# Optimization experiments

Measured on AMD Instinct MI355X. Metric: run time of the kernel, lower is better.

Reference implementation:

```python
import jax, jax.numpy as jnp
import numpy as np


def _conv3d(x, w, stride, pad):
    return jax.lax.conv_general_dilated(
        x, w, window_strides=stride, padding=[(p, p) for p in pad],
        dimension_numbers=('NCDHW', 'OIDHW', 'NCDHW'))


def _bn(x, g, b, eps=1e-5):
    # BatchNorm3d in training mode: batch statistics over (N, D, H, W)
    m = x.mean((0, 2, 3, 4), keepdims=True)
    v = ((x - m) ** 2).mean((0, 2, 3, 4), keepdims=True)
    return (x - m) * jax.lax.rsqrt(v + eps) * g.reshape(1, -1, 1, 1, 1) + b.reshape(1, -1, 1, 1, 1)


def _lrelu(x):
    return jnp.where(x >= 0, x, 0.2 * x)


def _deform_conv3d(x, off, w, stride, pad, n_off_groups):
    # Deformable conv3d: offsets predict per-output-location (dz,dy,dx) shifts for
    # every kernel tap, shared across channel groups of size C//n_off_groups.
    B, C, D, H, W = x.shape
    O, _, kd, kh, kw = w.shape
    K = kd * kh * kw
    sd, sh, sw = stride
    pd, ph, pw = pad
    Do = (D + 2 * pd - kd) // sd + 1
    Ho = (H + 2 * ph - kh) // sh + 1
    Wo = (W + 2 * pw - kw) // sw + 1
    G = n_off_groups
    Cg = C // G
    # offset layout: [B, G, K, 3(dz,dy,dx), Do, Ho, Wo]
    off = off.reshape(B, G, K, 3, Do, Ho, Wo)
    kz, ky, kx = jnp.meshgrid(jnp.arange(kd), jnp.arange(kh), jnp.arange(kw), indexing='ij')
    bz = (jnp.arange(Do) * sd - pd).astype(x.dtype)[:, None, None]
    by = (jnp.arange(Ho) * sh - ph).astype(x.dtype)[None, :, None]
    bx = (jnp.arange(Wo) * sw - pw).astype(x.dtype)[None, None, :]
    kb = lambda a: a.reshape(-1).astype(x.dtype)[None, None, :, None, None, None]
    pz = off[:, :, :, 0] + bz + kb(kz)   # [B,G,K,Do,Ho,Wo]
    py = off[:, :, :, 1] + by + kb(ky)
    px = off[:, :, :, 2] + bx + kb(kx)
    z0, y0, x0 = jnp.floor(pz), jnp.floor(py), jnp.floor(px)
    fz, fy, fx = pz - z0, py - y0, px - x0
    xg = x.reshape(B, G, Cg, D * H * W)
    acc = jnp.zeros((B, G, Cg, K, Do, Ho, Wo), x.dtype)
    for cz in (0, 1):
        for cy in (0, 1):
            for cx in (0, 1):
                zc, yc, xc = z0 + cz, y0 + cy, x0 + cx
                wgt = ((fz if cz else 1 - fz) * (fy if cy else 1 - fy) * (fx if cx else 1 - fx))
                valid = ((zc >= 0) & (zc <= D - 1) & (yc >= 0) & (yc <= H - 1)
                         & (xc >= 0) & (xc <= W - 1)).astype(x.dtype)
                zi = jnp.clip(zc, 0, D - 1).astype(jnp.int32)
                yi = jnp.clip(yc, 0, H - 1).astype(jnp.int32)
                xi = jnp.clip(xc, 0, W - 1).astype(jnp.int32)
                idx = ((zi * H + yi) * W + xi).reshape(B, G, 1, -1)
                v = jnp.take_along_axis(xg, jnp.broadcast_to(idx, (B, G, Cg, idx.shape[-1])), axis=3)
                acc = acc + (wgt * valid)[:, :, None] * v.reshape(B, G, Cg, K, Do, Ho, Wo)
    val = acc.reshape(B, C, K, Do, Ho, Wo)
    return jnp.einsum('bckdhw,ock->bodhw', val, w.reshape(O, C, K))


def setup_inputs() -> dict:
    key = jax.random.key(0)
    ks = jax.random.split(key, 24)
    f32 = jnp.float32
    p = lambda k, shape, s=0.05: jax.random.normal(k, shape, f32) * s
    gb = lambda k, c: (1.0 + 0.05 * jax.random.normal(k, (c,), f32),
                       0.05 * jax.random.normal(jax.random.fold_in(k, 1), (c,), f32))
    g2, b2 = gb(ks[8], 64)
    g3, b3 = gb(ks[9], 128)
    g4, b4 = gb(ks[10], 256)
    g5, b5 = gb(ks[11], 512)
    g6, b6 = gb(ks[12], 512)
    return {
        'input': jax.random.normal(ks[0], (64, 3, 8, 128, 128), f32),
        'w1': p(ks[1], (32, 3, 4, 4, 4)),
        'w2': p(ks[2], (64, 32, 2, 4, 4)),
        'w3': p(ks[3], (128, 64, 2, 4, 4)),
        'w4': p(ks[4], (256, 128, 1, 4, 4)),
        'w_off': p(ks[5], (192, 256, 1, 4, 4), 0.01),
        'w5': p(ks[6], (512, 256, 1, 4, 4)),
        'w6': p(ks[7], (512, 512, 1, 4, 4)),
        'g2': g2, 'b2': b2, 'g3': g3, 'b3': b3, 'g4': g4, 'b4': b4,
        'g5': g5, 'b5': b5, 'g6': g6, 'b6': b6,
    }


def reference(input, w1, w2, w3, w4, w_off, w5, w6,
              g2, b2, g3, b3, g4, b4, g5, b5, g6, b6):
    encs = []
    out = _lrelu(_conv3d(input, w1, (2, 2, 2), (1, 1, 1)))          # norm_1 unused in forward
    encs.append(out)
    out = _lrelu(_bn(_conv3d(out, w2, (1, 2, 2), (0, 1, 1)), g2, b2))
    encs.append(out)
    out = _lrelu(_bn(_conv3d(out, w3, (1, 2, 2), (0, 1, 1)), g3, b3))
    encs.append(out)
    out = _lrelu(_bn(_conv3d(out, w4, (1, 2, 2), (0, 1, 1)), g4, b4))
    encs.append(out)
    off = _conv3d(out, w_off, (1, 2, 2), (0, 1, 1))
    out = _lrelu(_bn(_deform_conv3d(out, off, w5, (1, 2, 2), (0, 1, 1), 4), g5, b5))
    encs.append(out)
    out = _lrelu(_bn(_conv3d(out, w6, (1, 1, 1), (0, 0, 0)), g6, b6))
    encs.append(out)
    return tuple(encs)
```

## Files before the change

kernel.cpp:

```cpp
#include <hip/hip_runtime.h>
#include <hip/hip_bf16.h>
#include <cstdint>

typedef short bf16x8 __attribute__((ext_vector_type(8)));
typedef float f32x4 __attribute__((ext_vector_type(4)));

__device__ __forceinline__ float lrelu_f(float y) { return y >= 0.f ? y : 0.2f * y; }
__device__ __forceinline__ float b2f(unsigned short u) {
    union { unsigned int i; float f; } v; v.i = ((unsigned int)u) << 16; return v.f;
}
__device__ __forceinline__ unsigned short f2b(float f) {
    union { unsigned int i; float f; } v; v.f = f;
    unsigned int r = v.i + 0x7FFFu + ((v.i >> 16) & 1u);
    return (unsigned short)(r >> 16);
}

__global__ __launch_bounds__(256) void xin_cl_k(const float* __restrict__ x,
                                                unsigned short* __restrict__ xc)
{
    int i = blockIdx.x * 256 + threadIdx.x;
    int c = i & 3, w = (i >> 2) & 127, h = (i >> 9) & 127, d = (i >> 16) & 7, b = i >> 19;
    float v = (c < 3) ? x[(((size_t)b * 3 + c) * 8 + d) * 16384 + h * 128 + w] : 0.f;
    xc[i] = f2b(v);
}

__global__ __launch_bounds__(256) void repack_w(const float* __restrict__ w,
                                                unsigned short* __restrict__ wp,
                                                int Cin, int Tap, int Cip, long total)
{
    long i = (long)blockIdx.x * 256 + threadIdx.x;
    if (i >= total) return;
    int c = (int)(i % Cip);
    long t1 = i / Cip;
    int t = (int)(t1 % Tap);
    long o = t1 / Tap;
    wp[i] = (c < Cin) ? f2b(w[((size_t)o * Cin + c) * Tap + t]) : (unsigned short)0;
}

__global__ __launch_bounds__(256) void f2bk(const float* __restrict__ in,
                                            unsigned short* __restrict__ o, long n)
{
    long i = (long)blockIdx.x * 256 + threadIdx.x;
    if (i < n) o[i] = f2b(in[i]);
}

template<int BN, int AMODE, int EPI>
__global__ __launch_bounds__(256) void igemm(
    const unsigned short* __restrict__ A, const unsigned short* __restrict__ Bw,
    void* __restrict__ Cout,
    int M, int N, int K, int klen,
    int Ci, int Di, int Hi, int Wi,
    int kd, int kh, int kw,
    int sd, int sh_, int sw_, int pd, int ph_, int pw_,
    int Do, int Ho, int Wo)
{
    constexpr int NF = BN / 32;
    constexpr int WN = 16 * NF;
    constexpr int NBU = (BN * 4 + 255) / 256;
    __shared__ __align__(16) unsigned short As[4][128][8];
    __shared__ __align__(16) unsigned short Bs[4][BN][8];
    const int tid = threadIdx.x;
    const int m0 = blockIdx.x * 128;
    const int n0 = blockIdx.y * BN;
    const int k0 = blockIdx.z * klen;
    const int kend = min(K, k0 + klen);

    size_t bsrc[NBU];
    unsigned short* bdst[NBU];
#pragma unroll
    for (int i = 0; i < NBU; ++i) {
        int u = tid + i * 256;
        int row = u >> 2, s = u & 3;
        if (BN * 4 >= 256 || u < BN * 4) {
            bsrc[i] = (size_t)(n0 + row) * K + s * 8;
            bdst[i] = &Bs[s][row][0];
        }
    }

    constexpr int NAU = (AMODE == 2) ? 4 : 2;
    size_t asz[2];
    int asrc[NAU];
    unsigned long long amask[NAU];
    unsigned short* adst[NAU];

    if constexpr (AMODE == 0) {
#pragma unroll
        for (int i = 0; i < 2; ++i) {
            int u = tid + i * 256;
            int r = u >> 2, s = u & 3;
            asz[i] = (size_t)(m0 + r) * K + s * 8;
            adst[i] = &As[s][r][0];
        }
    } else {
#pragma unroll
        for (int i = 0; i < NAU; ++i) {
            int u = tid + i * 256;
            int r = (AMODE == 2) ? (u >> 3) : (u >> 2);
            int m = m0 + r;
            int ow = m % Wo; int t1 = m / Wo;
            int oh = t1 % Ho; t1 /= Ho;
            int od = t1 % Do; int b = t1 / Do;
            int id0 = od * sd - pd, ih0 = oh * sh_ - ph_, iw0 = ow * sw_ - pw_;
            unsigned long long xm = 0ull, yx = 0ull, mask = 0ull;
            for (int p = 0; p < kw; ++p) if ((unsigned)(iw0 + p) < (unsigned)Wi) xm |= 1ull << p;
            for (int p = 0; p < kh; ++p) if ((unsigned)(ih0 + p) < (unsigned)Hi) yx |= xm << (p * kw);
            for (int p = 0; p < kd; ++p) if ((unsigned)(id0 + p) < (unsigned)Di) mask |= yx << (p * kh * kw);
            amask[i] = mask;
            int bsp = ((b * Di + id0) * Hi + ih0) * Wi + iw0;
            if constexpr (AMODE == 1) {
                int s = u & 3;
                asrc[i] = bsp * Ci + s * 8;
                adst[i] = &As[s][r][0];
            } else {
                int j = u & 7;
                asrc[i] = (bsp + (j >> 2) * Wi + (j & 3)) * 4;
                adst[i] = &As[j >> 1][r][(j & 1) * 4];
            }
        }
    }

    f32x4 acc[4][NF];
#pragma unroll
    for (int i = 0; i < 4; ++i)
#pragma unroll
        for (int j = 0; j < NF; ++j) acc[i][j] = (f32x4){0.f, 0.f, 0.f, 0.f};

    const int lane = tid & 63, wv = tid >> 6;
    const int wm = wv >> 1, wn = wv & 1;
    const int kg = lane >> 4, fr = lane & 15;

    int c0 = 0, kx = 0, ky = 0, tap = 0, doff = 0;
    if constexpr (AMODE == 1) {
        c0 = k0 % Ci;
        tap = k0 / Ci;
        kx = tap % kw;
        int t2 = tap / kw;
        ky = t2 % kh;
        int kz = t2 / kh;
        doff = (kz * Hi + ky) * Wi + kx;
    }

    for (int k = k0; k < kend; k += 32) {
#pragma unroll
        for (int i = 0; i < NBU; ++i)
            if (BN * 4 >= 256 || tid + i * 256 < BN * 4) {
                uint4 v = *(const uint4*)&Bw[bsrc[i] + k];
                *(uint4*)bdst[i] = v;
            }
        if constexpr (AMODE == 0) {
#pragma unroll
            for (int i = 0; i < 2; ++i) {
                uint4 v = *(const uint4*)&A[asz[i] + k];
                *(uint4*)adst[i] = v;
            }
        } else if constexpr (AMODE == 1) {
            int dofe = doff * Ci + c0;
#pragma unroll
            for (int i = 0; i < 2; ++i) {
                uint4 v = {0u, 0u, 0u, 0u};
                if ((amask[i] >> tap) & 1ull)
                    v = *(const uint4*)&A[(size_t)(asrc[i] + dofe)];
                *(uint4*)adst[i] = v;
            }
        } else {
            int kz = k >> 6;
            int U4 = (kz * (Hi * Wi) + ((k >> 5) & 1) * 2 * Wi) * 4;
            int tap0 = k >> 2;
#pragma unroll
            for (int i = 0; i < 4; ++i) {
                int j = (tid + i * 256) & 7;
                uint2 v = {0u, 0u};
                if ((amask[i] >> (tap0 + j)) & 1ull)
                    v = *(const uint2*)&A[(size_t)(asrc[i] + U4)];
                *(uint2*)adst[i] = v;
            }
        }
        __syncthreads();
        bf16x8 af[4], bfr[NF];
#pragma unroll
        for (int mi = 0; mi < 4; ++mi)
            af[mi] = *(const bf16x8*)&As[kg][wm * 64 + mi * 16 + fr][0];
#pragma unroll
        for (int ni = 0; ni < NF; ++ni)
            bfr[ni] = *(const bf16x8*)&Bs[kg][wn * WN + ni * 16 + fr][0];
#pragma unroll
        for (int mi = 0; mi < 4; ++mi)
#pragma unroll
            for (int ni = 0; ni < NF; ++ni)
                acc[mi][ni] = __builtin_amdgcn_mfma_f32_16x16x32_bf16(af[mi], bfr[ni], acc[mi][ni], 0, 0, 0);
        __syncthreads();
        if constexpr (AMODE == 1) {
            c0 += 32;
            if (c0 >= Ci) {
                c0 = 0; ++tap; ++kx; ++doff;
                if (kx == kw) {
                    kx = 0; doff += Wi - kw; ++ky;
                    if (ky == kh) { ky = 0; doff += (Hi - kh) * Wi; }
                }
            }
        }
    }
    const int rb = m0 + wm * 64 + (lane >> 4) * 4;
    const int cb = n0 + wn * WN + fr;
#pragma unroll
    for (int mi = 0; mi < 4; ++mi)
#pragma unroll
        for (int ni = 0; ni < NF; ++ni)
#pragma unroll
            for (int rg = 0; rg < 4; ++rg) {
                size_t idx = (size_t)(rb + mi * 16 + rg) * N + cb + ni * 16;
                float vv = acc[mi][ni][rg];
                if constexpr (EPI == 0) ((unsigned short*)Cout)[idx] = f2b(vv);
                else if constexpr (EPI == 1) ((float*)Cout)[idx] = vv;
                else if constexpr (EPI == 2) atomicAdd((float*)Cout + idx, vv);
                else ((unsigned short*)Cout)[idx] = f2b(lrelu_f(vv));
            }
}

__global__ __launch_bounds__(256) void bn_sums(const unsigned short* __restrict__ x,
                                               float* __restrict__ sums,
                                               long totalSlots, int C)
{
    const int tid = threadIdx.x;
    long gid = (long)blockIdx.x * 256 + tid;
    long stride = (long)gridDim.x * 256;
    float s1[8], s2[8];
#pragma unroll
    for (int j = 0; j < 8; ++j) { s1[j] = 0.f; s2[j] = 0.f; }
    for (long s = gid; s < totalSlots; s += stride) {
        uint4 v = *(const uint4*)&x[s * 8];
        const unsigned short* pv = (const unsigned short*)&v;
#pragma unroll
        for (int j = 0; j < 8; ++j) { float f = b2f(pv[j]); s1[j] += f; s2[j] += f * f; }
    }
    __shared__ float r1[2048], r2[2048];
#pragma unroll
    for (int j = 0; j < 8; ++j) { r1[tid * 8 + j] = s1[j]; r2[tid * 8 + j] = s2[j]; }
    __syncthreads();
    int G = C >> 3;
    for (int c = tid; c < C; c += 256) {
        int grp = c >> 3, j = c & 7;
        float a = 0.f, b = 0.f;
        for (int th = grp; th < 256; th += G) { a += r1[th * 8 + j]; b += r2[th * 8 + j]; }
        atomicAdd(&sums[c], a);
        atomicAdd(&sums[C + c], b);
    }
}

__global__ __launch_bounds__(256) void bn_fin(const float* __restrict__ sums,
                                              const float* __restrict__ g, const float* __restrict__ bt,
                                              float* __restrict__ sc, float* __restrict__ sh,
                                              int C, float invcnt)
{
    int c = blockIdx.x * 256 + threadIdx.x;
    if (c >= C) return;
    float mean = sums[c] * invcnt;
    float var = sums[C + c] * invcnt - mean * mean;
    float rs = rsqrtf(var + 1e-5f);
    float scl = g[c] * rs;
    sc[c] = scl;
    sh[c] = bt[c] - mean * scl;
}

template<int MODE>
__global__ __launch_bounds__(256) void bn_apply_t(
    unsigned short* __restrict__ x, const float* __restrict__ sc, const float* __restrict__ sh,
    float* __restrict__ outN, int C, int TC, int S)
{
    __shared__ __align__(16) float T[64][68];
    const int tid = threadIdx.x;
    const long m0 = (long)blockIdx.x * 64;
    const int c0 = blockIdx.y * TC;
    const int spr = TC >> 3;
    const int lg = (spr == 8) ? 3 : 2;
    const int tot = 64 * spr;
    for (int u = tid; u < tot; u += 256) {
        int r = u >> lg, sl = u & (spr - 1);
        size_t idx = (size_t)(m0 + r) * C + c0 + sl * 8;
        uint4 v = *(uint4*)&x[idx];
        unsigned short* pv = (unsigned short*)&v;
#pragma unroll
        for (int j = 0; j < 8; ++j) {
            int c = c0 + sl * 8 + j;
            float f = b2f(pv[j]);
            if (MODE == 1) {
                f = lrelu_f(f * sc[c] + sh[c]);
                pv[j] = f2b(f);
            }
            T[sl * 8 + j][r] = f;
        }
        if (MODE == 1) *(uint4*)&x[idx] = v;
    }
    __syncthreads();
    const int tpc = 256 / TC;
    const int rpt = 64 / tpc;
    int cl = tid / tpc;
    int r0 = (tid % tpc) * rpt;
    int c = c0 + cl;
    if ((S & 63) == 0) {
        long b = m0 / S;
        long s0 = m0 - b * S;
        float* op = outN + ((size_t)b * C + c) * S + s0 + r0;
        for (int r = 0; r < rpt; r += 4)
            *(float4*)(op + r) = *(float4*)&T[cl][r0 + r];
    } else {
        for (int r = 0; r < rpt; ++r) {
            long m = m0 + r0 + r;
            long b = m / S, s = m - b * S;
            outN[((size_t)b * C + c) * S + s] = T[cl][r0 + r];
        }
    }
}

__global__ __launch_bounds__(256) void deform_val(
    const unsigned short* __restrict__ xcl, const float* __restrict__ offc,
    unsigned short* __restrict__ val)
{
    int bs = blockIdx.x;
    int b = bs >> 5, s = bs & 31;
    int od = s >> 4, oh = (s >> 2) & 3, ow = s & 3;
    __shared__ float cw[64][8];
    __shared__ int cidx[64][8];
    int tid = threadIdx.x;
    if (tid < 64) {
        int gk = tid, k = gk & 15;
        int ky = k >> 2, kx = k & 3;
        const float* op = offc + (size_t)bs * 192 + gk * 3;
        float pz = op[0] + (float)od;
        float py = op[1] + (float)(oh * 2 - 1 + ky);
        float px = op[2] + (float)(ow * 2 - 1 + kx);
        float z0 = floorf(pz), y0 = floorf(py), x0 = floorf(px);
        float fz = pz - z0, fy = py - y0, fx = px - x0;
#pragma unroll
        for (int ci = 0; ci < 8; ++ci) {
            int cz = ci >> 2, cy = (ci >> 1) & 1, cx = ci & 1;
            float zc = z0 + cz, yc = y0 + cy, xc = x0 + cx;
            bool ok = zc >= 0.f && zc <= 1.f && yc >= 0.f && yc <= 7.f && xc >= 0.f && xc <= 7.f;
            int zi = min(max((int)zc, 0), 1);
            int yi = min(max((int)yc, 0), 7);
            int xi = min(max((int)xc, 0), 7);
            float wz = cz ? fz : 1.f - fz;
            float wy = cy ? fy : 1.f - fy;
            float wx = cx ? fx : 1.f - fx;
            cw[gk][ci] = ok ? wz * wy * wx : 0.f;
            cidx[gk][ci] = (zi * 8 + yi) * 8 + xi;
        }
    }
    __syncthreads();
    const unsigned short* xb = xcl + (size_t)b * 128 * 256;
    unsigned short* vo = val + (size_t)bs * 4096;
    for (int j = tid; j < 4096; j += 256) {
        int c = j & 255, tap = j >> 8;
        int gk = ((c >> 6) << 4) | tap;
        float v = 0.f;
#pragma unroll
        for (int i = 0; i < 8; ++i)
            v += cw[gk][i] * b2f(xb[(size_t)cidx[gk][i] * 256 + c]);
        vo[j] = f2b(v);
    }
}

extern "C" void kernel_launch(void* const* d_in, const int* in_sizes, int n_in,
                              void* d_out, int out_size, void* d_ws, size_t ws_size,
                              hipStream_t stream)
{
    (void)in_sizes; (void)n_in; (void)out_size; (void)ws_size;
    const float* x     = (const float*)d_in[0];
    const float* w1    = (const float*)d_in[1];
    const float* w2    = (const float*)d_in[2];
    const float* w3    = (const float*)d_in[3];
    const float* w4    = (const float*)d_in[4];
    const float* w_off = (const float*)d_in[5];
    const float* w5    = (const float*)d_in[6];
    const float* w6    = (const float*)d_in[7];
    const float* g2 = (const float*)d_in[8];  const float* b2 = (const float*)d_in[9];
    const float* g3 = (const float*)d_in[10]; const float* b3 = (const float*)d_in[11];
    const float* g4 = (const float*)d_in[12]; const float* b4 = (const float*)d_in[13];
    const float* g5 = (const float*)d_in[14]; const float* b5 = (const float*)d_in[15];
    const float* g6 = (const float*)d_in[16]; const float* b6 = (const float*)d_in[17];

    float* out = (float*)d_out;
    float* enc0 = out;
    float* enc1 = out + 33554432;
    float* enc2 = out + 46137344;
    float* enc3 = out + 50331648;
    float* enc4 = out + 52428800;
    float* enc5 = out + 53477376;

    char* W = (char*)d_ws;
    unsigned short* w1p  = (unsigned short*)(W + 0);
    unsigned short* w2p  = (unsigned short*)(W + 16384);
    unsigned short* w3p  = (unsigned short*)(W + 147456);
    unsigned short* w4p  = (unsigned short*)(W + 671744);
    unsigned short* wofp = (unsigned short*)(W + 1720320);
    unsigned short* w5p  = (unsigned short*)(W + 3293184);
    unsigned short* w6p  = (unsigned short*)(W + 7487488);
    float* sums          = (float*)(W + 15876096);
    float* sc            = (float*)(W + 15880192);
    float* sh            = (float*)(W + 15882240);
    float* offc          = (float*)(W + 15884288);
    unsigned short* xcl  = (unsigned short*)(W + 17457152);
    unsigned short* e1c  = (unsigned short*)(W + 17457152);
    unsigned short* e2c  = (unsigned short*)(W + 42622976);
    unsigned short* e3c  = (unsigned short*)(W + 51011584);
    unsigned short* e0c  = (unsigned short*)(W + 84566016);
    unsigned short* valb = (unsigned short*)(W + 84566016);
    float* raw5          = (float*)(W + 101343232);
    unsigned short* e4c  = (unsigned short*)(W + 105537536);
    float* raw6          = (float*)(W + 107634688);
    unsigned short* e5c  = (unsigned short*)(W + 107896832);

    xin_cl_k<<<131072, 256, 0, stream>>>(x, xcl);
    repack_w<<<32, 256, 0, stream>>>(w1, w1p, 3, 64, 4, 8192L);
    repack_w<<<256, 256, 0, stream>>>(w2, w2p, 32, 32, 32, 65536L);
    repack_w<<<1024, 256, 0, stream>>>(w3, w3p, 64, 32, 64, 262144L);
    repack_w<<<2048, 256, 0, stream>>>(w4, w4p, 128, 16, 128, 524288L);
    repack_w<<<3072, 256, 0, stream>>>(w_off, wofp, 256, 16, 256, 786432L);
    repack_w<<<8192, 256, 0, stream>>>(w5, w5p, 256, 16, 256, 2097152L);
    repack_w<<<16384, 256, 0, stream>>>(w6, w6p, 512, 16, 512, 4194304L);

    igemm<32, 2, 3><<<dim3(8192, 1, 1), 256, 0, stream>>>(
        xcl, w1p, e0c, 1048576, 32, 256, 256,
        4, 8, 128, 128, 4, 4, 4, 2, 2, 2, 1, 1, 1, 4, 64, 64);
    bn_apply_t<0><<<dim3(16384, 1), 256, 0, stream>>>(e0c, nullptr, nullptr, enc0, 32, 32, 16384);

    igemm<64, 1, 0><<<dim3(1536, 1, 1), 256, 0, stream>>>(
        e0c, w2p, e1c, 196608, 64, 1024, 1024,
        32, 4, 64, 64, 2, 4, 4, 1, 2, 2, 0, 1, 1, 3, 32, 32);
    hipMemsetAsync(sums, 0, 4096, stream);
    bn_sums<<<256, 256, 0, stream>>>(e1c, sums, 1572864L, 64);
    bn_fin<<<1, 256, 0, stream>>>(sums, g2, b2, sc, sh, 64, 1.f / 196608.f);
    bn_apply_t<1><<<dim3(3072, 1), 256, 0, stream>>>(e1c, sc, sh, enc1, 64, 64, 3072);

    igemm<128, 1, 0><<<dim3(256, 1, 1), 256, 0, stream>>>(
        e1c, w3p, e2c, 32768, 128, 2048, 2048,
        64, 3, 32, 32, 2, 4, 4, 1, 2, 2, 0, 1, 1, 2, 16, 16);
    hipMemsetAsync(sums, 0, 4096, stream);
    bn_sums<<<256, 256, 0, stream>>>(e2c, sums, 524288L, 128);
    bn_fin<<<1, 256, 0, stream>>>(sums, g3, b3, sc, sh, 128, 1.f / 32768.f);
    bn_apply_t<1><<<dim3(512, 2), 256, 0, stream>>>(e2c, sc, sh, enc2, 128, 64, 512);

    igemm<64, 1, 0><<<dim3(64, 4), 256, 0, stream>>>(
        e2c, w4p, e3c, 8192, 256, 2048, 2048,
        128, 2, 16, 16, 1, 4, 4, 1, 2, 2, 0, 1, 1, 2, 8, 8);
    hipMemsetAsync(sums, 0, 4096, stream);
    bn_sums<<<256, 256, 0, stream>>>(e3c, sums, 262144L, 256);
    bn_fin<<<1, 256, 0, stream>>>(sums, g4, b4, sc, sh, 256, 1.f / 8192.f);
    bn_apply_t<1><<<dim3(128, 4), 256, 0, stream>>>(e3c, sc, sh, enc3, 256, 64, 128);

    hipMemsetAsync(offc, 0, 1572864, stream);
    igemm<64, 1, 2><<<dim3(16, 3, 8), 256, 0, stream>>>(
        e3c, wofp, offc, 2048, 192, 4096, 512,
        256, 2, 8, 8, 1, 4, 4, 1, 2, 2, 0, 1, 1, 2, 4, 4);

    deform_val<<<2048, 256, 0, stream>>>(e3c, offc, valb);
    hipMemsetAsync(raw5, 0, 4194304, stream);
    igemm<64, 0, 2><<<dim3(16, 8, 4), 256, 0, stream>>>(
        valb, w5p, raw5, 2048, 512, 4096, 1024,
        0, 0, 0, 0, 1, 1, 1, 1, 1, 1, 0, 0, 0, 1, 1, 1);
    f2bk<<<4096, 256, 0, stream>>>(raw5, e4c, 1048576L);
    hipMemsetAsync(sums, 0, 4096, stream);
    bn_sums<<<256, 256, 0, stream>>>(e4c, sums, 131072L, 512);
    bn_fin<<<2, 256, 0, stream>>>(sums, g5, b5, sc, sh, 512, 1.f / 2048.f);
    bn_apply_t<1><<<dim3(32, 8), 256, 0, stream>>>(e4c, sc, sh, enc4, 512, 64, 32);

    hipMemsetAsync(raw6, 0, 262144, stream);
    igemm<64, 0, 2><<<dim3(1, 8, 16), 256, 0, stream>>>(
        e4c, w6p, raw6, 128, 512, 8192, 512,
        0, 0, 0, 0, 1, 1, 1, 1, 1, 1, 0, 0, 0, 1, 1, 1);
    f2bk<<<256, 256, 0, stream>>>(raw6, e5c, 65536L);
    hipMemsetAsync(sums, 0, 4096, stream);
    bn_sums<<<256, 256, 0, stream>>>(e5c, sums, 8192L, 512);
    bn_fin<<<2, 256, 0, stream>>>(sums, g6, b6, sc, sh, 512, 1.f / 128.f);
    bn_apply_t<1><<<dim3(2, 8), 256, 0, stream>>>(e5c, sc, sh, enc5, 512, 64, 2);
}
```

Measured before the change: 650.2 us.

## Fuse BN statistics into GEMM epilogue, merge weight repacks, unroll K by 64

The seven weight-repack launches become one kernel. BN sum and sum-of-squares are now accumulated in the igemm epilogue (new EPI mode 4), using shared-memory reduction and then global atomics, which removes the separate bn_sums passes and most memsets; bn_fin now zeroes the sums for the next layer. The f32-to-bf16 conversion and the stats are fused into one pass for the split-K layers. The GEMM main loop now stages two 32-wide K slices per sync, halving barriers, and the split-K factor is doubled for layers 5 and 6. In exchange it uses more shared memory per block and adds atomic contention in the epilogue, and the BN stats are now computed from fp32 values rather than from the rounded bf16 outputs.

```diff
diff --git a/kernel.cpp b/kernel.cpp
--- a/kernel.cpp
+++ b/kernel.cpp
@@ -24,30 +24,32 @@
     xc[i] = f2b(v);
 }
 
-__global__ __launch_bounds__(256) void repack_w(const float* __restrict__ w,
-                                                unsigned short* __restrict__ wp,
-                                                int Cin, int Tap, int Cip, long total)
+__global__ __launch_bounds__(256) void repack_all(
+    const float* __restrict__ w1, const float* __restrict__ w2,
+    const float* __restrict__ w3, const float* __restrict__ w4,
+    const float* __restrict__ w_off, const float* __restrict__ w5,
+    const float* __restrict__ w6, unsigned short* __restrict__ wp)
 {
     long i = (long)blockIdx.x * 256 + threadIdx.x;
-    if (i >= total) return;
-    int c = (int)(i % Cip);
-    long t1 = i / Cip;
+    const float* src; int Cin, Tap, Cip; long rel;
+    if (i < 8192)         { src = w1;    Cin = 3;   Tap = 64; Cip = 4;   rel = i; }
+    else if (i < 73728)   { src = w2;    Cin = 32;  Tap = 32; Cip = 32;  rel = i - 8192; }
+    else if (i < 335872)  { src = w3;    Cin = 64;  Tap = 32; Cip = 64;  rel = i - 73728; }
+    else if (i < 860160)  { src = w4;    Cin = 128; Tap = 16; Cip = 128; rel = i - 335872; }
+    else if (i < 1646592) { src = w_off; Cin = 256; Tap = 16; Cip = 256; rel = i - 860160; }
+    else if (i < 3743744) { src = w5;    Cin = 256; Tap = 16; Cip = 256; rel = i - 1646592; }
+    else                  { src = w6;    Cin = 512; Tap = 16; Cip = 512; rel = i - 3743744; }
+    int c = (int)(rel % Cip);
+    long t1 = rel / Cip;
     int t = (int)(t1 % Tap);
     long o = t1 / Tap;
-    wp[i] = (c < Cin) ? f2b(w[((size_t)o * Cin + c) * Tap + t]) : (unsigned short)0;
-}
-
-__global__ __launch_bounds__(256) void f2bk(const float* __restrict__ in,
-                                            unsigned short* __restrict__ o, long n)
-{
-    long i = (long)blockIdx.x * 256 + threadIdx.x;
-    if (i < n) o[i] = f2b(in[i]);
+    wp[i] = (c < Cin) ? f2b(src[((size_t)o * Cin + c) * Tap + t]) : (unsigned short)0;
 }
 
 template<int BN, int AMODE, int EPI>
 __global__ __launch_bounds__(256) void igemm(
     const unsigned short* __restrict__ A, const unsigned short* __restrict__ Bw,
-    void* __restrict__ Cout,
+    void* __restrict__ Cout, float* __restrict__ sums,
     int M, int N, int K, int klen,
     int Ci, int Di, int Hi, int Wi,
     int kd, int kh, int kw,
@@ -57,31 +59,36 @@
     constexpr int NF = BN / 32;
     constexpr int WN = 16 * NF;
     constexpr int NBU = (BN * 4 + 255) / 256;
-    __shared__ __align__(16) unsigned short As[4][128][8];
-    __shared__ __align__(16) unsigned short Bs[4][BN][8];
+    constexpr int NAU = (AMODE == 2) ? 4 : 2;
+    constexpr int ASTR = 4 * 128 * 8;
+    constexpr int BSTR = 4 * BN * 8;
+    __shared__ __align__(16) unsigned short As[2][4][128][8];
+    __shared__ __align__(16) unsigned short Bs[2][4][BN][8];
+    __shared__ float redbuf[(EPI == 4) ? 2 * BN : 1];
     const int tid = threadIdx.x;
     const int m0 = blockIdx.x * 128;
     const int n0 = blockIdx.y * BN;
     const int k0 = blockIdx.z * klen;
     const int kend = min(K, k0 + klen);
+    unsigned short* const As0 = &As[0][0][0][0];
+    unsigned short* const Bs0 = &Bs[0][0][0][0];
 
     size_t bsrc[NBU];
-    unsigned short* bdst[NBU];
+    int boff[NBU];
 #pragma unroll
     for (int i = 0; i < NBU; ++i) {
         int u = tid + i * 256;
         int row = u >> 2, s = u & 3;
         if (BN * 4 >= 256 || u < BN * 4) {
             bsrc[i] = (size_t)(n0 + row) * K + s * 8;
-            bdst[i] = &Bs[s][row][0];
-        }
-    }
-
-    constexpr int NAU = (AMODE == 2) ? 4 : 2;
+            boff[i] = (s * BN + row) * 8;
+        }
+    }
+
     size_t asz[2];
     int asrc[NAU];
     unsigned long long amask[NAU];
-    unsigned short* adst[NAU];
+    int aoff[NAU];
 
     if constexpr (AMODE == 0) {
 #pragma unroll
@@ -89,7 +96,7 @@
             int u = tid + i * 256;
             int r = u >> 2, s = u & 3;
             asz[i] = (size_t)(m0 + r) * K + s * 8;
-            adst[i] = &As[s][r][0];
+            aoff[i] = (s * 128 + r) * 8;
         }
     } else {
 #pragma unroll
@@ -110,11 +117,11 @@
             if constexpr (AMODE == 1) {
                 int s = u & 3;
                 asrc[i] = bsp * Ci + s * 8;
-                adst[i] = &As[s][r][0];
+                aoff[i] = (s * 128 + r) * 8;
             } else {
                 int j = u & 7;
                 asrc[i] = (bsp + (j >> 2) * Wi + (j & 3)) * 4;
-                adst[i] = &As[j >> 1][r][(j & 1) * 4];
+                aoff[i] = ((j >> 1) * 128 + r) * 8 + (j & 1) * 4;
             }
         }
     }
@@ -139,87 +146,132 @@
         int kz = t2 / kh;
         doff = (kz * Hi + ky) * Wi + kx;
     }
-
-    for (int k = k0; k < kend; k += 32) {
+    auto advance = [&]() {
+        c0 += 32;
+        if (c0 >= Ci) {
+            c0 = 0; ++tap; ++kx; ++doff;
+            if (kx == kw) {
+                kx = 0; doff += Wi - kw; ++ky;
+                if (ky == kh) { ky = 0; doff += (Hi - kh) * Wi; }
+            }
+        }
+    };
+
+    for (int k = k0; k < kend; k += 64) {
 #pragma unroll
         for (int i = 0; i < NBU; ++i)
             if (BN * 4 >= 256 || tid + i * 256 < BN * 4) {
-                uint4 v = *(const uint4*)&Bw[bsrc[i] + k];
-                *(uint4*)bdst[i] = v;
+                uint4 v0 = *(const uint4*)&Bw[bsrc[i] + k];
+                uint4 v1 = *(const uint4*)&Bw[bsrc[i] + k + 32];
+                *(uint4*)(Bs0 + boff[i]) = v0;
+                *(uint4*)(Bs0 + BSTR + boff[i]) = v1;
             }
         if constexpr (AMODE == 0) {
 #pragma unroll
             for (int i = 0; i < 2; ++i) {
-                uint4 v = *(const uint4*)&A[asz[i] + k];
-                *(uint4*)adst[i] = v;
+                uint4 v0 = *(const uint4*)&A[asz[i] + k];
+                uint4 v1 = *(const uint4*)&A[asz[i] + k + 32];
+                *(uint4*)(As0 + aoff[i]) = v0;
+                *(uint4*)(As0 + ASTR + aoff[i]) = v1;
             }
         } else if constexpr (AMODE == 1) {
-            int dofe = doff * Ci + c0;
+            int t0 = tap, d0 = doff * Ci + c0;
+            advance();
+            int t1 = tap, d1 = doff * Ci + c0;
+            advance();
 #pragma unroll
             for (int i = 0; i < 2; ++i) {
-                uint4 v = {0u, 0u, 0u, 0u};
-                if ((amask[i] >> tap) & 1ull)
-                    v = *(const uint4*)&A[(size_t)(asrc[i] + dofe)];
-                *(uint4*)adst[i] = v;
+                uint4 v0 = {0u, 0u, 0u, 0u}, v1 = {0u, 0u, 0u, 0u};
+                if ((amask[i] >> t0) & 1ull) v0 = *(const uint4*)&A[(size_t)(asrc[i] + d0)];
+                if ((amask[i] >> t1) & 1ull) v1 = *(const uint4*)&A[(size_t)(asrc[i] + d1)];
+                *(uint4*)(As0 + aoff[i]) = v0;
+                *(uint4*)(As0 + ASTR + aoff[i]) = v1;
             }
         } else {
             int kz = k >> 6;
-            int U4 = (kz * (Hi * Wi) + ((k >> 5) & 1) * 2 * Wi) * 4;
+            int U0 = kz * (Hi * Wi) * 4;
+            int U1 = U0 + 2 * Wi * 4;
             int tap0 = k >> 2;
 #pragma unroll
             for (int i = 0; i < 4; ++i) {
                 int j = (tid + i * 256) & 7;
-                uint2 v = {0u, 0u};
+                uint2 v0 = {0u, 0u}, v1 = {0u, 0u};
                 if ((amask[i] >> (tap0 + j)) & 1ull)
-                    v = *(const uint2*)&A[(size_t)(asrc[i] + U4)];
-                *(uint2*)adst[i] = v;
+                    v0 = *(const uint2*)&A[(size_t)(asrc[i] + U0)];
+                if ((amask[i] >> (tap0 + 8 + j)) & 1ull)
+                    v1 = *(const uint2*)&A[(size_t)(asrc[i] + U1)];
+                *(uint2*)(As0 + aoff[i]) = v0;
+                *(uint2*)(As0 + ASTR + aoff[i]) = v1;
             }
         }
         __syncthreads();
-        bf16x8 af[4], bfr[NF];
-#pragma unroll
-        for (int mi = 0; mi < 4; ++mi)
-            af[mi] = *(const bf16x8*)&As[kg][wm * 64 + mi * 16 + fr][0];
-#pragma unroll
-        for (int ni = 0; ni < NF; ++ni)
-            bfr[ni] = *(const bf16x8*)&Bs[kg][wn * WN + ni * 16 + fr][0];
-#pragma unroll
-        for (int mi = 0; mi < 4; ++mi)
+#pragma unroll
+        for (int kb = 0; kb < 2; ++kb) {
+            bf16x8 af[4], bfr[NF];
+#pragma unroll
+            for (int mi = 0; mi < 4; ++mi)
+                af[mi] = *(const bf16x8*)&As[kb][kg][wm * 64 + mi * 16 + fr][0];
 #pragma unroll
             for (int ni = 0; ni < NF; ++ni)
-                acc[mi][ni] = __builtin_amdgcn_mfma_f32_16x16x32_bf16(af[mi], bfr[ni], acc[mi][ni], 0, 0, 0);
+                bfr[ni] = *(const bf16x8*)&Bs[kb][kg][wn * WN + ni * 16 + fr][0];
+#pragma unroll
+            for (int mi = 0; mi < 4; ++mi)
+#pragma unroll
+                for (int ni = 0; ni < NF; ++ni)
+                    acc[mi][ni] = __builtin_amdgcn_mfma_f32_16x16x32_bf16(af[mi], bfr[ni], acc[mi][ni], 0, 0, 0);
+        }
         __syncthreads();
-        if constexpr (AMODE == 1) {
-            c0 += 32;
-            if (c0 >= Ci) {
-                c0 = 0; ++tap; ++kx; ++doff;
-                if (kx == kw) {
-                    kx = 0; doff += Wi - kw; ++ky;
-                    if (ky == kh) { ky = 0; doff += (Hi - kh) * Wi; }
-                }
-            }
-        }
+    }
+
+    if constexpr (EPI == 4) {
+        for (int j = tid; j < 2 * BN; j += 256) redbuf[j] = 0.f;
+        __syncthreads();
     }
     const int rb = m0 + wm * 64 + (lane >> 4) * 4;
     const int cb = n0 + wn * WN + fr;
+    float p1[NF], p2[NF];
+    if constexpr (EPI == 4) {
+#pragma unroll
+        for (int ni = 0; ni < NF; ++ni) { p1[ni] = 0.f; p2[ni] = 0.f; }
+    }
 #pragma unroll
     for (int mi = 0; mi < 4; ++mi)
 #pragma unroll
-        for (int ni = 0; ni < NF; ++ni)
-#pragma unroll
-            for (int rg = 0; rg < 4; ++rg) {
-                size_t idx = (size_t)(rb + mi * 16 + rg) * N + cb + ni * 16;
+        for (int rg = 0; rg < 4; ++rg) {
+            size_t rowbase = (size_t)(rb + mi * 16 + rg) * N;
+#pragma unroll
+            for (int ni = 0; ni < NF; ++ni) {
+                size_t idx = rowbase + cb + ni * 16;
                 float vv = acc[mi][ni][rg];
                 if constexpr (EPI == 0) ((unsigned short*)Cout)[idx] = f2b(vv);
                 else if constexpr (EPI == 1) ((float*)Cout)[idx] = vv;
                 else if constexpr (EPI == 2) atomicAdd((float*)Cout + idx, vv);
-                else ((unsigned short*)Cout)[idx] = f2b(lrelu_f(vv));
-            }
-}
-
-__global__ __launch_bounds__(256) void bn_sums(const unsigned short* __restrict__ x,
-                                               float* __restrict__ sums,
-                                               long totalSlots, int C)
+                else if constexpr (EPI == 3) ((unsigned short*)Cout)[idx] = f2b(lrelu_f(vv));
+                else {
+                    ((unsigned short*)Cout)[idx] = f2b(vv);
+                    p1[ni] += vv; p2[ni] += vv * vv;
+                }
+            }
+        }
+    if constexpr (EPI == 4) {
+#pragma unroll
+        for (int ni = 0; ni < NF; ++ni) {
+            int cl = wn * WN + ni * 16 + fr;
+            atomicAdd(&redbuf[cl], p1[ni]);
+            atomicAdd(&redbuf[BN + cl], p2[ni]);
+        }
+        __syncthreads();
+        for (int j = tid; j < 2 * BN; j += 256) {
+            int gcol = (j < BN) ? (n0 + j) : (N + n0 + j - BN);
+            atomicAdd(&sums[gcol], redbuf[j]);
+        }
+    }
+}
+
+__global__ __launch_bounds__(256) void f2b_sums(const float* __restrict__ in,
+                                                unsigned short* __restrict__ o,
+                                                float* __restrict__ sums,
+                                                long totalSlots, int C)
 {
     const int tid = threadIdx.x;
     long gid = (long)blockIdx.x * 256 + tid;
@@ -228,10 +280,13 @@
 #pragma unroll
     for (int j = 0; j < 8; ++j) { s1[j] = 0.f; s2[j] = 0.f; }
     for (long s = gid; s < totalSlots; s += stride) {
-        uint4 v = *(const uint4*)&x[s * 8];
-        const unsigned short* pv = (const unsigned short*)&v;
-#pragma unroll
-        for (int j = 0; j < 8; ++j) { float f = b2f(pv[j]); s1[j] += f; s2[j] += f * f; }
+        float4 a = *(const float4*)&in[s * 8];
+        float4 b = *(const float4*)&in[s * 8 + 4];
+        float f[8] = {a.x, a.y, a.z, a.w, b.x, b.y, b.z, b.w};
+        unsigned short u[8];
+#pragma unroll
+        for (int j = 0; j < 8; ++j) { u[j] = f2b(f[j]); s1[j] += f[j]; s2[j] += f[j] * f[j]; }
+        *(uint4*)&o[s * 8] = *(uint4*)u;
     }
     __shared__ float r1[2048], r2[2048];
 #pragma unroll
@@ -247,7 +302,7 @@
     }
 }
 
-__global__ __launch_bounds__(256) void bn_fin(const float* __restrict__ sums,
+__global__ __launch_bounds__(256) void bn_fin(float* __restrict__ sums,
                                               const float* __restrict__ g, const float* __restrict__ bt,
                                               float* __restrict__ sc, float* __restrict__ sh,
                                               int C, float invcnt)
@@ -260,6 +315,8 @@
     float scl = g[c] * rs;
     sc[c] = scl;
     sh[c] = bt[c] - mean * scl;
+    sums[c] = 0.f;
+    sums[C + c] = 0.f;
 }
 
 template<int MODE>
@@ -388,6 +445,7 @@
     float* enc5 = out + 53477376;
 
     char* W = (char*)d_ws;
+    unsigned short* wpk  = (unsigned short*)(W + 0);
     unsigned short* w1p  = (unsigned short*)(W + 0);
     unsigned short* w2p  = (unsigned short*)(W + 16384);
     unsigned short* w3p  = (unsigned short*)(W + 147456);
@@ -410,67 +468,52 @@
     float* raw6          = (float*)(W + 107634688);
     unsigned short* e5c  = (unsigned short*)(W + 107896832);
 
+    hipMemsetAsync(sums, 0, 4096, stream);
     xin_cl_k<<<131072, 256, 0, stream>>>(x, xcl);
-    repack_w<<<32, 256, 0, stream>>>(w1, w1p, 3, 64, 4, 8192L);
-    repack_w<<<256, 256, 0, stream>>>(w2, w2p, 32, 32, 32, 65536L);
-    repack_w<<<1024, 256, 0, stream>>>(w3, w3p, 64, 32, 64, 262144L);
-    repack_w<<<2048, 256, 0, stream>>>(w4, w4p, 128, 16, 128, 524288L);
-    repack_w<<<3072, 256, 0, stream>>>(w_off, wofp, 256, 16, 256, 786432L);
-    repack_w<<<8192, 256, 0, stream>>>(w5, w5p, 256, 16, 256, 2097152L);
-    repack_w<<<16384, 256, 0, stream>>>(w6, w6p, 512, 16, 512, 4194304L);
+    repack_all<<<31008, 256, 0, stream>>>(w1, w2, w3, w4, w_off, w5, w6, wpk);
 
     igemm<32, 2, 3><<<dim3(8192, 1, 1), 256, 0, stream>>>(
-        xcl, w1p, e0c, 1048576, 32, 256, 256,
+        xcl, w1p, e0c, nullptr, 1048576, 32, 256, 256,
         4, 8, 128, 128, 4, 4, 4, 2, 2, 2, 1, 1, 1, 4, 64, 64);
     bn_apply_t<0><<<dim3(16384, 1), 256, 0, stream>>>(e0c, nullptr, nullptr, enc0, 32, 32, 16384);
 
-    igemm<64, 1, 0><<<dim3(1536, 1, 1), 256, 0, stream>>>(
-        e0c, w2p, e1c, 196608, 64, 1024, 1024,
+    igemm<64, 1, 4><<<dim3(1536, 1, 1), 256, 0, stream>>>(
+        e0c, w2p, e1c, sums, 196608, 64, 1024, 1024,
         32, 4, 64, 64, 2, 4, 4, 1, 2, 2, 0, 1, 1, 3, 32, 32);
-    hipMemsetAsync(sums, 0, 4096, stream);
-    bn_sums<<<256, 256, 0, stream>>>(e1c, sums, 1572864L, 64);
     bn_fin<<<1, 256, 0, stream>>>(sums, g2, b2, sc, sh, 64, 1.f / 196608.f);
     bn_apply_t<1><<<dim3(3072, 1), 256, 0, stream>>>(e1c, sc, sh, enc1, 64, 64, 3072);
 
-    igemm<128, 1, 0><<<dim3(256, 1, 1), 256, 0, stream>>>(
-        e1c, w3p, e2c, 32768, 128, 2048, 2048,
+    igemm<128, 1, 4><<<dim3(256, 1, 1), 256, 0, stream>>>(
+        e1c, w3p, e2c, sums, 32768, 128, 2048, 2048,
         64, 3, 32, 32, 2, 4, 4, 1, 2, 2, 0, 1, 1, 2, 16, 16);
-    hipMemsetAsync(sums, 0, 4096, stream);
-    bn_sums<<<256, 256, 0, stream>>>(e2c, sums, 524288L, 128);
     bn_fin<<<1, 256, 0, stream>>>(sums, g3, b3, sc, sh, 128, 1.f / 32768.f);
     bn_apply_t<1><<<dim3(512, 2), 256, 0, stream>>>(e2c, sc, sh, enc2, 128, 64, 512);
 
-    igemm<64, 1, 0><<<dim3(64, 4), 256, 0, stream>>>(
-        e2c, w4p, e3c, 8192, 256, 2048, 2048,
+    igemm<64, 1, 4><<<dim3(64, 4), 256, 0, stream>>>(
+        e2c, w4p, e3c, sums, 8192, 256, 2048, 2048,
         128, 2, 16, 16, 1, 4, 4, 1, 2, 2, 0, 1, 1, 2, 8, 8);
-    hipMemsetAsync(sums, 0, 4096, stream);
-    bn_sums<<<256, 256, 0, stream>>>(e3c, sums, 262144L, 256);
     bn_fin<<<1, 256, 0, stream>>>(sums, g4, b4, sc, sh, 256, 1.f / 8192.f);
     bn_apply_t<1><<<dim3(128, 4), 256, 0, stream>>>(e3c, sc, sh, enc3, 256, 64, 128);
 
     hipMemsetAsync(offc, 0, 1572864, stream);
     igemm<64, 1, 2><<<dim3(16, 3, 8), 256, 0, stream>>>(
-        e3c, wofp, offc, 2048, 192, 4096, 512,
+        e3c, wofp, offc, nullptr, 2048, 192, 4096, 512,
         256, 2, 8, 8, 1, 4, 4, 1, 2, 2, 0, 1, 1, 2, 4, 4);
 
     deform_val<<<2048, 256, 0, stream>>>(e3c, offc, valb);
     hipMemsetAsync(raw5, 0, 4194304, stream);
-    igemm<64, 0, 2><<<dim3(16, 8, 4), 256, 0, stream>>>(
-        valb, w5p, raw5, 2048, 512, 4096, 1024,
+    igemm<64, 0, 2><<<dim3(16, 8, 8), 256, 0, stream>>>(
+        valb, w5p, raw5, nullptr, 2048, 512, 4096, 512,
         0, 0, 0, 0, 1, 1, 1, 1, 1, 1, 0, 0, 0, 1, 1, 1);
-    f2bk<<<4096, 256, 0, stream>>>(raw5, e4c, 1048576L);
-    hipMemsetAsync(sums, 0, 4096, stream);
-    bn_sums<<<256, 256, 0, stream>>>(e4c, sums, 131072L, 512);
+    f2b_sums<<<256, 256, 0, stream>>>(raw5, e4c, sums, 131072L, 512);
     bn_fin<<<2, 256, 0, stream>>>(sums, g5, b5, sc, sh, 512, 1.f / 2048.f);
     bn_apply_t<1><<<dim3(32, 8), 256, 0, stream>>>(e4c, sc, sh, enc4, 512, 64, 32);
 
     hipMemsetAsync(raw6, 0, 262144, stream);
-    igemm<64, 0, 2><<<dim3(1, 8, 16), 256, 0, stream>>>(
-        e4c, w6p, raw6, 128, 512, 8192, 512,
+    igemm<64, 0, 2><<<dim3(1, 8, 32), 256, 0, stream>>>(
+        e4c, w6p, raw6, nullptr, 128, 512, 8192, 256,
         0, 0, 0, 0, 1, 1, 1, 1, 1, 1, 0, 0, 0, 1, 1, 1);
-    f2bk<<<256, 256, 0, stream>>>(raw6, e5c, 65536L);
-    hipMemsetAsync(sums, 0, 4096, stream);
-    bn_sums<<<256, 256, 0, stream>>>(e5c, sums, 8192L, 512);
+    f2b_sums<<<32, 256, 0, stream>>>(raw6, e5c, sums, 8192L, 512);
     bn_fin<<<2, 256, 0, stream>>>(sums, g6, b6, sc, sh, 512, 1.f / 128.f);
     bn_apply_t<1><<<dim3(2, 8), 256, 0, stream>>>(e5c, sc, sh, enc5, 512, 64, 2);
 }
```

Measured after the change: 586.4 us. 9.8% less time.
